# Kernel tuning notes

Measured on AMD Instinct MI355X. Metric: run time of the kernel, lower is better.

The kernel has to match this reference:

```python
import jax, jax.numpy as jnp
import numpy as np

NB_STEPS = 50  # quadrature steps (51 Clenshaw-Curtis nodes)
IN_D = 8
HIDDEN = [256, 256, 256]
B = 8192


def _cc_quadrature(nb_steps):
    # Clenshaw-Curtis weights/nodes, exactly as in UMNN's ParallelNeuralIntegral
    lam = np.arange(nb_steps + 1).reshape(-1, 1)
    lam = np.cos((lam @ lam.T) * np.pi / nb_steps)
    lam[:, 0] = 0.5
    lam[:, -1] = 0.5 * lam[:, -1]
    lam = lam * 2.0 / nb_steps
    W = np.arange(nb_steps + 1).reshape(-1, 1)
    W[np.arange(1, nb_steps + 1, 2)] = 0
    W = 2.0 / (1 - W.astype(np.float64) ** 2)
    W[0] = 1.0
    W[np.arange(1, nb_steps + 1, 2)] = 0.0
    cc_weights = (lam.T @ W).astype(np.float32)  # [S+1, 1]
    steps = np.cos(np.arange(nb_steps + 1).reshape(-1, 1) * np.pi / nb_steps).astype(np.float32)  # [S+1,1]
    return jnp.asarray(cc_weights), jnp.asarray(steps)


def setup_inputs() -> dict:
    key = jax.random.key(0)
    ks = jax.random.split(key, 20)
    inp = {
        "x": jax.random.normal(ks[0], (B, 1), dtype=jnp.float32),
        "h": jax.random.normal(ks[1], (B, IN_D - 1), dtype=jnp.float32),
    }
    # integrand net: in_d -> 256 -> 256 -> 256 -> 1
    i_dims = [IN_D] + HIDDEN + [1]
    for li, (d0, d1) in enumerate(zip(i_dims, i_dims[1:])):
        scale = 1.0 / np.sqrt(d0)
        inp[f"iW{li}"] = jax.random.uniform(ks[2 + li], (d0, d1), jnp.float32, -scale, scale)
        inp[f"ib{li}"] = jax.random.uniform(ks[6 + li], (d1,), jnp.float32, -scale, scale)
    # h net: (in_d-1) -> 256 -> 256 -> 256 -> 2
    h_dims = [IN_D - 1] + HIDDEN + [2]
    for li, (d0, d1) in enumerate(zip(h_dims, h_dims[1:])):
        scale = 1.0 / np.sqrt(d0)
        inp[f"hW{li}"] = jax.random.uniform(ks[10 + li], (d0, d1), jnp.float32, -scale, scale)
        inp[f"hb{li}"] = jax.random.uniform(ks[14 + li], (d1,), jnp.float32, -scale, scale)
    return inp


def _integrand(z, Ws, bs):
    # IntegrandNN: Linear+ReLU chain, final Linear+ELU, then +1
    for W, b in zip(Ws[:-1], bs[:-1]):
        z = jax.nn.relu(z @ W + b)
    return jax.nn.elu(z @ Ws[-1] + bs[-1]) + 1.0


def _hnet(z, Ws, bs):
    # Linear+ReLU chain, final Linear (ReLU popped)
    for W, b in zip(Ws[:-1], bs[:-1]):
        z = jax.nn.relu(z @ W + b)
    return z @ Ws[-1] + bs[-1]


def _forward(x, h, iWs, ibs, hWs, hbs):
    cc_w, steps = _cc_quadrature(NB_STEPS)  # [S,1], [S,1]
    S = NB_STEPS + 1
    b = x.shape[0]
    # quadrature nodes mapped from [-1,1] to [0, x] (x0 = 0)
    X = x[:, None, :] * (steps[None, :, :] + 1.0) * 0.5          # [B,S,1]
    Hs = jnp.broadcast_to(h[:, None, :], (b, S, h.shape[1]))     # [B,S,in_d-1]
    z = jnp.concatenate([X, Hs], axis=-1)                        # [B,S,in_d]
    dz = _integrand(z, iWs, ibs)                                 # [B,S,1]
    integral = jnp.sum(dz * cc_w[None, :, :], axis=1) * x * 0.5  # [B,1]
    out = _hnet(h, hWs, hbs)                                     # [B,2]
    offset = out[:, :1]
    scaling = jnp.exp(out[:, 1:2])
    return scaling * integral + offset


def reference(x, h, iW0, ib0, iW1, ib1, iW2, ib2, iW3, ib3,
              hW0, hb0, hW1, hb1, hW2, hb2, hW3, hb3):
    iWs = [iW0, iW1, iW2, iW3]
    ibs = [ib0, ib1, ib2, ib3]
    hWs = [hW0, hW1, hW2, hW3]
    hbs = [hb0, hb1, hb2, hb3]
    return _forward(x, h, iWs, ibs, hWs, hbs)
```

## Files before the change

### kernel.cpp

```cpp
#include <hip/hip_runtime.h>
#include <hip/hip_bf16.h>
#include <math.h>

using bf16x8 = __attribute__((ext_vector_type(8))) __bf16;
using f32x16 = __attribute__((ext_vector_type(16))) float;

#define B_SZ    8192
#define S_STEPS 51
#define M_ROWS  (B_SZ * S_STEPS)
#define TROWS   64

__device__ __forceinline__ f32x16 mfma32(bf16x8 a, bf16x8 b, f32x16 c) {
    return __builtin_amdgcn_mfma_f32_32x32x16_bf16(a, b, c, 0, 0, 0);
}

__global__ void ccq_kernel(float* __restrict__ ccw, float* __restrict__ stp) {
    int s = threadIdx.x;
    if (s >= S_STEPS) return;
    double pi50 = M_PI / 50.0;
    double acc = 0.0;
    for (int j = 0; j <= 50; j += 2) {
        double wq = (j == 0) ? 1.0 : 2.0 / (1.0 - (double)(j * j));
        double m;
        if (s == 0) m = 0.5;
        else if (s == 50) m = 0.5;
        else m = cos((double)(j * s) * pi50);
        acc += m * wq;
    }
    ccw[s] = (float)(acc * (2.0 / 50.0));
    stp[s] = (float)cos((double)s * pi50);
}

struct PackArgs {
    const float* src[8];
    __hip_bfloat16* dst[8];
    int Ks[8], Ns[8], KST[8], perm[8];
    int prefix[9];
};

__global__ void pack_all(PackArgs pa) {
    int idx = blockIdx.x * 256 + threadIdx.x;
    if (idx >= pa.prefix[8]) return;
    int m = 0;
    while (idx >= pa.prefix[m + 1]) ++m;
    int e = idx - pa.prefix[m];
    int KST = pa.KST[m];
    int j    = e & 7;
    int lane = (e >> 3) & 63;
    int ks   = (e >> 9) % KST;
    int cg   = (e >> 9) / KST;
    int col = cg * 32 + (lane & 31);
    int k   = ks * 16 + (lane >> 5) * 8 + j;
    int kk  = pa.perm[m] ? ((k & ~63) | (((k & 63) >> 1) + 32 * (k & 1))) : k;
    float v = (kk < pa.Ks[m] && col < pa.Ns[m]) ? pa.src[m][kk * pa.Ns[m] + col] : 0.0f;
    ((__bf16*)pa.dst[m])[e] = (__bf16)v;
}


template<int KST, int CHUNKS, int MASK>
__device__ __forceinline__ void gemm_compute(const __bf16* __restrict__ actIn,
                                             const __bf16* __restrict__ wpack,
                                             f32x16 (&acc)[2][2],
                                             int wc, int lane) {
    const bf16x8* wp = (const bf16x8*)wpack;
    const int la = lane & 31, hi = lane >> 5;
#pragma unroll 4
    for (int ks = 0; ks < KST; ++ks) {
        bf16x8 b0 = wp[((wc * 2 + 0) * KST + ks) * 64 + lane];
        bf16x8 b1 = wp[((wc * 2 + 1) * KST + ks) * 64 + lane];
        int chunk = ks * 2 + hi;
#pragma unroll
        for (int m = 0; m < 2; ++m) {
            int row = m * 32 + la;
            bf16x8 af = *(const bf16x8*)(actIn + (row * CHUNKS + (chunk ^ (row & MASK))) * 8);
            acc[m][0] = mfma32(af, b0, acc[m][0]);
            acc[m][1] = mfma32(af, b1, acc[m][1]);
        }
    }
}

__device__ __forceinline__ void epilogue_store(f32x16 (&acc)[2][2],
                                               const float* __restrict__ bias,
                                               __bf16* __restrict__ actOut,
                                               int wc, int lane) {
    const int la = lane & 31, hi = lane >> 5;
    unsigned* dst = (unsigned*)actOut;
    int F = wc * 64 + la;
    float b0 = bias[F], b1 = bias[F + 32];
    int d = wc * 32 + la;
    int c = d >> 2, w = d & 3;
#pragma unroll
    for (int m = 0; m < 2; ++m) {
#pragma unroll
        for (int r = 0; r < 16; ++r) {
            int row = m * 32 + (r & 3) + 8 * (r >> 2) + 4 * hi;
            float v0 = fmaxf(acc[m][0][r] + b0, 0.0f);
            float v1 = fmaxf(acc[m][1][r] + b1, 0.0f);
            union { __bf16 h2[2]; unsigned u; } cv;
            cv.h2[0] = (__bf16)v0; cv.h2[1] = (__bf16)v1;
            dst[(row * 32 + (c ^ (row & 31))) * 4 + w] = cv.u;
        }
    }
}

template<int MODE>
__device__ __forceinline__ void final_layer(const __bf16* __restrict__ actIn,
                                            const __bf16* __restrict__ wpack,
                                            const float* __restrict__ bias,
                                            float* __restrict__ out0,
                                            float* __restrict__ out1,
                                            int rb, int wid, int lane) {
    const bf16x8* wp = (const bf16x8*)wpack;
    const int la = lane & 31, hi = lane >> 5;
    f32x16 acc = (f32x16)0.0f;
    int row = wid * 32 + la;
#pragma unroll 4
    for (int ks = 0; ks < 16; ++ks) {
        int chunk = ks * 2 + hi;
        bf16x8 af = *(const bf16x8*)(actIn + (row * 32 + (chunk ^ (row & 31))) * 8);
        acc = mfma32(af, wp[ks * 64 + lane], acc);
    }
    if (MODE == 0) {
        if (la == 0) {
            float b = bias[0];
#pragma unroll
            for (int r = 0; r < 16; ++r) {
                int rr = wid * 32 + (r & 3) + 8 * (r >> 2) + 4 * hi;
                float v = acc[r] + b;
                out0[rb + rr] = (v > 0.0f) ? (v + 1.0f) : expf(v);
            }
        }
    } else {
        if (la < 2) {
            float b = bias[la];
            float* dst = (la == 0) ? out0 : out1;
#pragma unroll
            for (int r = 0; r < 16; ++r) {
                int rr = wid * 32 + (r & 3) + 8 * (r >> 2) + 4 * hi;
                dst[rb + rr] = acc[r] + b;
            }
        }
    }
}

template<int MODE>
__global__ __launch_bounds__(256, 4) void mlp_kernel(
    const float* __restrict__ x, const float* __restrict__ h,
    const float* __restrict__ steps,
    const __bf16* __restrict__ w0p, const __bf16* __restrict__ w1p,
    const __bf16* __restrict__ w2p, const __bf16* __restrict__ w3p,
    const float* __restrict__ b0, const float* __restrict__ b1,
    const float* __restrict__ b2, const float* __restrict__ b3,
    float* __restrict__ out0, float* __restrict__ out1) {
    __shared__ __bf16 act[TROWS * 256];
    __shared__ __bf16 zin[TROWS * 32];

    int tid  = threadIdx.x;
    int lane = tid & 63;
    int wid  = tid >> 6;
    int wc   = wid;
    int rb   = blockIdx.x * TROWS;

    {
        int row   = tid >> 2;
        int cpart = tid & 3;
        float vals[8];
        if (MODE == 0) {
            int s  = rb >> 13;
            int i  = (rb & (B_SZ - 1)) + row;
            float sc = (steps[s] + 1.0f) * 0.5f;
#pragma unroll
            for (int j = 0; j < 8; ++j) {
                int c = cpart * 8 + j;
                float v = 0.0f;
                if (c == 0) v = x[i] * sc;
                else if (c < 8) v = h[i * 7 + c - 1];
                vals[j] = v;
            }
        } else {
            int i = rb + row;
#pragma unroll
            for (int j = 0; j < 8; ++j) {
                int c = cpart * 8 + j;
                vals[j] = (c < 7) ? h[i * 7 + c] : 0.0f;
            }
        }
        bf16x8 zv;
#pragma unroll
        for (int j = 0; j < 8; ++j) zv[j] = (__bf16)vals[j];
        int zidx = (row * 4 + (cpart ^ (row & 3))) * 8;
        *(bf16x8*)(zin + zidx) = zv;
    }
    __syncthreads();

    f32x16 acc[2][2];

#pragma unroll
    for (int m = 0; m < 2; ++m)
#pragma unroll
        for (int n = 0; n < 2; ++n) acc[m][n] = (f32x16)0.0f;
    gemm_compute<2, 4, 3>(zin, w0p, acc, wc, lane);
    epilogue_store(acc, b0, act, wc, lane);
    __syncthreads();

#pragma unroll
    for (int m = 0; m < 2; ++m)
#pragma unroll
        for (int n = 0; n < 2; ++n) acc[m][n] = (f32x16)0.0f;
    gemm_compute<16, 32, 31>(act, w1p, acc, wc, lane);
    __syncthreads();
    epilogue_store(acc, b1, act, wc, lane);
    __syncthreads();

#pragma unroll
    for (int m = 0; m < 2; ++m)
#pragma unroll
        for (int n = 0; n < 2; ++n) acc[m][n] = (f32x16)0.0f;
    gemm_compute<16, 32, 31>(act, w2p, acc, wc, lane);
    __syncthreads();
    epilogue_store(acc, b2, act, wc, lane);
    __syncthreads();

    if (wid < 2)
        final_layer<MODE>(act, w3p, b3, out0, out1, rb, wid, lane);
}

__global__ void reduce_kernel(const float* __restrict__ dz, const float* __restrict__ x,
                              const float* __restrict__ ho, const float* __restrict__ hs,
                              const float* __restrict__ ccw, float* __restrict__ out) {
    __shared__ float w[S_STEPS];
    int t = threadIdx.x;
    if (t < S_STEPS) w[t] = ccw[t];
    __syncthreads();
    int i = blockIdx.x * blockDim.x + t;
    float acc = 0.0f;
    for (int s = 0; s < S_STEPS; ++s) acc += dz[s * B_SZ + i] * w[s];
    float integral = acc * x[i] * 0.5f;
    out[i] = expf(hs[i]) * integral + ho[i];
}

extern "C" void kernel_launch(void* const* d_in, const int* in_sizes, int n_in,
                              void* d_out, int out_size, void* d_ws, size_t ws_size,
                              hipStream_t stream) {
    (void)in_sizes; (void)n_in; (void)out_size; (void)ws_size;
    const float* x = (const float*)d_in[0];
    const float* h = (const float*)d_in[1];
    const float* iW[4] = {(const float*)d_in[2], (const float*)d_in[4],
                          (const float*)d_in[6], (const float*)d_in[8]};
    const float* ib[4] = {(const float*)d_in[3], (const float*)d_in[5],
                          (const float*)d_in[7], (const float*)d_in[9]};
    const float* hW[4] = {(const float*)d_in[10], (const float*)d_in[12],
                          (const float*)d_in[14], (const float*)d_in[16]};
    const float* hb[4] = {(const float*)d_in[11], (const float*)d_in[13],
                          (const float*)d_in[15], (const float*)d_in[17]};

    size_t off = 0;
    auto alloc = [&](size_t bytes) -> void* {
        void* p = (char*)d_ws + off;
        off += (bytes + 255) & ~(size_t)255;
        return p;
    };
    float*  dz   = (float*)alloc((size_t)M_ROWS * 4);
    float*  ho   = (float*)alloc(B_SZ * 4);
    float*  hs   = (float*)alloc(B_SZ * 4);
    float*  ccw  = (float*)alloc(64 * 4);
    float*  stp  = (float*)alloc(64 * 4);
    __bf16* iW0p = (__bf16*)alloc(8 * 2 * 512 * 2);
    __bf16* iW1p = (__bf16*)alloc(8 * 16 * 512 * 2);
    __bf16* iW2p = (__bf16*)alloc(8 * 16 * 512 * 2);
    __bf16* iW3p = (__bf16*)alloc(1 * 16 * 512 * 2);
    __bf16* hW0p = (__bf16*)alloc(8 * 2 * 512 * 2);
    __bf16* hW1p = (__bf16*)alloc(8 * 16 * 512 * 2);
    __bf16* hW2p = (__bf16*)alloc(8 * 16 * 512 * 2);
    __bf16* hW3p = (__bf16*)alloc(1 * 16 * 512 * 2);

    ccq_kernel<<<1, 64, 0, stream>>>(ccw, stp);

    PackArgs pa;
    const float* srcs[8] = {iW[0], iW[1], iW[2], iW[3], hW[0], hW[1], hW[2], hW[3]};
    __bf16*      dsts[8] = {iW0p, iW1p, iW2p, iW3p, hW0p, hW1p, hW2p, hW3p};
    int Ks[8]  = {8, 256, 256, 256, 7, 256, 256, 256};
    int Ns[8]  = {256, 256, 256, 1, 256, 256, 256, 2};
    int KST[8] = {2, 16, 16, 16, 2, 16, 16, 16};
    int CG[8]  = {8, 8, 8, 1, 8, 8, 8, 1};
    int PM[8]  = {0, 1, 1, 1, 0, 1, 1, 1};
    int pfx = 0;
    for (int m = 0; m < 8; ++m) {
        pa.src[m] = srcs[m];
        pa.dst[m] = (__hip_bfloat16*)dsts[m];
        pa.Ks[m] = Ks[m]; pa.Ns[m] = Ns[m]; pa.KST[m] = KST[m]; pa.perm[m] = PM[m];
        pa.prefix[m] = pfx;
        pfx += CG[m] * KST[m] * 512;
    }
    pa.prefix[8] = pfx;
    pack_all<<<(pfx + 255) / 256, 256, 0, stream>>>(pa);

    mlp_kernel<0><<<M_ROWS / TROWS, 256, 0, stream>>>(
        x, h, stp, iW0p, iW1p, iW2p, iW3p, ib[0], ib[1], ib[2], ib[3], dz, dz);
    mlp_kernel<1><<<B_SZ / TROWS, 256, 0, stream>>>(
        x, h, stp, hW0p, hW1p, hW2p, hW3p, hb[0], hb[1], hb[2], hb[3], ho, hs);

    reduce_kernel<<<B_SZ / 256, 256, 0, stream>>>(dz, x, ho, hs, ccw, (float*)d_out);
}
```

Measured before the change: 163.3 us.

## Load first-layer inputs directly into MFMA registers and precompute LDS swizzle offsets

The first layer no longer stages its inputs through a shared-memory tile. Each lane now loads x and h straight from global memory into bf16 MFMA fragments, and the layer uses a single K-step, which removes one barrier and the zin buffer. The hidden-layer GEMM and epilogue address shared memory through precomputed byte offsets with an XOR swizzle, the k-loop is fully unrolled, and wave priority is raised around the MFMA loop. The aim is less address arithmetic, fewer LDS round trips and better MFMA issue, at the cost of more registers and half the lanes sitting idle during the layer-0 load.

```diff
diff --git a/kernel.cpp b/kernel.cpp
--- a/kernel.cpp
+++ b/kernel.cpp
@@ -57,26 +57,66 @@
 }
 
 
-template<int KST, int CHUNKS, int MASK>
+template<int KST>
 __device__ __forceinline__ void gemm_compute(const __bf16* __restrict__ actIn,
                                              const __bf16* __restrict__ wpack,
                                              f32x16 (&acc)[2][2],
                                              int wc, int lane) {
     const bf16x8* wp = (const bf16x8*)wpack;
     const int la = lane & 31, hi = lane >> 5;
-#pragma unroll 4
+    const char* base = (const char*)actIn;
+    const int C0 = la * 512 + ((hi ^ (la & 1)) << 4);
+    const int D  = (la & 30) << 4;
+    __builtin_amdgcn_s_setprio(1);
+#pragma unroll
     for (int ks = 0; ks < KST; ++ks) {
         bf16x8 b0 = wp[((wc * 2 + 0) * KST + ks) * 64 + lane];
         bf16x8 b1 = wp[((wc * 2 + 1) * KST + ks) * 64 + lane];
-        int chunk = ks * 2 + hi;
-#pragma unroll
-        for (int m = 0; m < 2; ++m) {
+        const int kv = ks << 5;
+        bf16x8 a0 = *(const bf16x8*)(base + C0 + (kv ^ D));
+        bf16x8 a1 = *(const bf16x8*)(base + C0 + 16384 + (kv ^ D));
+        acc[0][0] = mfma32(a0, b0, acc[0][0]);
+        acc[0][1] = mfma32(a0, b1, acc[0][1]);
+        acc[1][0] = mfma32(a1, b0, acc[1][0]);
+        acc[1][1] = mfma32(a1, b1, acc[1][1]);
+    }
+    __builtin_amdgcn_s_setprio(0);
+}
+
+template<int MODE>
+__device__ __forceinline__ void l0_compute(const float* __restrict__ x,
+                                           const float* __restrict__ h,
+                                           float sc,
+                                           const __bf16* __restrict__ w0p,
+                                           f32x16 (&acc)[2][2],
+                                           int rb, int wc, int lane) {
+    const bf16x8* wp = (const bf16x8*)w0p;
+    const int la = lane & 31, hi = lane >> 5;
+    bf16x8 a[2];
+#pragma unroll
+    for (int m = 0; m < 2; ++m) {
+        bf16x8 v = (bf16x8)(__bf16)0.0f;
+        if (hi == 0) {
             int row = m * 32 + la;
-            bf16x8 af = *(const bf16x8*)(actIn + (row * CHUNKS + (chunk ^ (row & MASK))) * 8);
-            acc[m][0] = mfma32(af, b0, acc[m][0]);
-            acc[m][1] = mfma32(af, b1, acc[m][1]);
+            int i = (MODE == 0) ? ((rb & (B_SZ - 1)) + row) : (rb + row);
+            const float* hp = h + i * 7;
+            if (MODE == 0) {
+                v[0] = (__bf16)(x[i] * sc);
+#pragma unroll
+                for (int j = 0; j < 7; ++j) v[j + 1] = (__bf16)hp[j];
+            } else {
+#pragma unroll
+                for (int j = 0; j < 7; ++j) v[j] = (__bf16)hp[j];
+            }
         }
-    }
+        a[m] = v;
+    }
+    bf16x8 b0 = wp[(wc * 2 + 0) * 64 + lane];
+    bf16x8 b1 = wp[(wc * 2 + 1) * 64 + lane];
+    acc[0][0] = mfma32(a[0], b0, acc[0][0]);
+    acc[0][1] = mfma32(a[0], b1, acc[0][1]);
+    acc[1][0] = mfma32(a[1], b0, acc[1][0]);
+    acc[1][1] = mfma32(a[1], b1, acc[1][1]);
 }
 
 __device__ __forceinline__ void epilogue_store(f32x16 (&acc)[2][2],
@@ -84,21 +124,22 @@
                                                __bf16* __restrict__ actOut,
                                                int wc, int lane) {
     const int la = lane & 31, hi = lane >> 5;
-    unsigned* dst = (unsigned*)actOut;
+    char* dst = (char*)actOut;
     int F = wc * 64 + la;
-    float b0 = bias[F], b1 = bias[F + 32];
+    float b0v = bias[F], b1v = bias[F + 32];
     int d = wc * 32 + la;
-    int c = d >> 2, w = d & 3;
+    const int cH4 = ((d >> 2) ^ (hi << 2)) << 4;
+    const int P   = hi * 2048 + ((d & 3) << 2);
 #pragma unroll
     for (int m = 0; m < 2; ++m) {
 #pragma unroll
         for (int r = 0; r < 16; ++r) {
-            int row = m * 32 + (r & 3) + 8 * (r >> 2) + 4 * hi;
-            float v0 = fmaxf(acc[m][0][r] + b0, 0.0f);
-            float v1 = fmaxf(acc[m][1][r] + b1, 0.0f);
+            const int K_r = (r & 3) + 8 * (r >> 2);
+            float v0 = fmaxf(acc[m][0][r] + b0v, 0.0f);
+            float v1 = fmaxf(acc[m][1][r] + b1v, 0.0f);
             union { __bf16 h2[2]; unsigned u; } cv;
             cv.h2[0] = (__bf16)v0; cv.h2[1] = (__bf16)v1;
-            dst[(row * 32 + (c ^ (row & 31))) * 4 + w] = cv.u;
+            *(unsigned*)(dst + P + m * 16384 + K_r * 512 + (cH4 ^ (K_r << 4))) = cv.u;
         }
     }
 }
@@ -112,12 +153,13 @@
                                             int rb, int wid, int lane) {
     const bf16x8* wp = (const bf16x8*)wpack;
     const int la = lane & 31, hi = lane >> 5;
+    const char* base = (const char*)actIn;
+    const int C = (wid * 32 + la) * 512 + ((hi ^ (la & 1)) << 4);
+    const int D = (la & 30) << 4;
     f32x16 acc = (f32x16)0.0f;
-    int row = wid * 32 + la;
-#pragma unroll 4
+#pragma unroll
     for (int ks = 0; ks < 16; ++ks) {
-        int chunk = ks * 2 + hi;
-        bf16x8 af = *(const bf16x8*)(actIn + (row * 32 + (chunk ^ (row & 31))) * 8);
+        bf16x8 af = *(const bf16x8*)(base + C + ((ks << 5) ^ D));
         acc = mfma32(af, wp[ks * 64 + lane], acc);
     }
     if (MODE == 0) {
@@ -153,7 +195,6 @@
     const float* __restrict__ b2, const float* __restrict__ b3,
     float* __restrict__ out0, float* __restrict__ out1) {
     __shared__ __bf16 act[TROWS * 256];
-    __shared__ __bf16 zin[TROWS * 32];
 
     int tid  = threadIdx.x;
     int lane = tid & 63;
@@ -161,37 +202,8 @@
     int wc   = wid;
     int rb   = blockIdx.x * TROWS;
 
-    {
-        int row   = tid >> 2;
-        int cpart = tid & 3;
-        float vals[8];
-        if (MODE == 0) {
-            int s  = rb >> 13;
-            int i  = (rb & (B_SZ - 1)) + row;
-            float sc = (steps[s] + 1.0f) * 0.5f;
-#pragma unroll
-            for (int j = 0; j < 8; ++j) {
-                int c = cpart * 8 + j;
-                float v = 0.0f;
-                if (c == 0) v = x[i] * sc;
-                else if (c < 8) v = h[i * 7 + c - 1];
-                vals[j] = v;
-            }
-        } else {
-            int i = rb + row;
-#pragma unroll
-            for (int j = 0; j < 8; ++j) {
-                int c = cpart * 8 + j;
-                vals[j] = (c < 7) ? h[i * 7 + c] : 0.0f;
-            }
-        }
-        bf16x8 zv;
-#pragma unroll
-        for (int j = 0; j < 8; ++j) zv[j] = (__bf16)vals[j];
-        int zidx = (row * 4 + (cpart ^ (row & 3))) * 8;
-        *(bf16x8*)(zin + zidx) = zv;
-    }
-    __syncthreads();
+    float sc = 0.0f;
+    if (MODE == 0) sc = (steps[rb >> 13] + 1.0f) * 0.5f;
 
     f32x16 acc[2][2];
 
@@ -199,7 +211,7 @@
     for (int m = 0; m < 2; ++m)
 #pragma unroll
         for (int n = 0; n < 2; ++n) acc[m][n] = (f32x16)0.0f;
-    gemm_compute<2, 4, 3>(zin, w0p, acc, wc, lane);
+    l0_compute<MODE>(x, h, sc, w0p, acc, rb, wc, lane);
     epilogue_store(acc, b0, act, wc, lane);
     __syncthreads();
 
@@ -207,7 +219,7 @@
     for (int m = 0; m < 2; ++m)
 #pragma unroll
         for (int n = 0; n < 2; ++n) acc[m][n] = (f32x16)0.0f;
-    gemm_compute<16, 32, 31>(act, w1p, acc, wc, lane);
+    gemm_compute<16>(act, w1p, acc, wc, lane);
     __syncthreads();
     epilogue_store(acc, b1, act, wc, lane);
     __syncthreads();
@@ -216,7 +228,7 @@
     for (int m = 0; m < 2; ++m)
 #pragma unroll
         for (int n = 0; n < 2; ++n) acc[m][n] = (f32x16)0.0f;
-    gemm_compute<16, 32, 31>(act, w2p, acc, wc, lane);
+    gemm_compute<16>(act, w2p, acc, wc, lane);
     __syncthreads();
     epilogue_store(acc, b2, act, wc, lane);
     __syncthreads();
@@ -265,11 +277,11 @@
     float*  hs   = (float*)alloc(B_SZ * 4);
     float*  ccw  = (float*)alloc(64 * 4);
     float*  stp  = (float*)alloc(64 * 4);
-    __bf16* iW0p = (__bf16*)alloc(8 * 2 * 512 * 2);
+    __bf16* iW0p = (__bf16*)alloc(8 * 1 * 512 * 2);
     __bf16* iW1p = (__bf16*)alloc(8 * 16 * 512 * 2);
     __bf16* iW2p = (__bf16*)alloc(8 * 16 * 512 * 2);
     __bf16* iW3p = (__bf16*)alloc(1 * 16 * 512 * 2);
-    __bf16* hW0p = (__bf16*)alloc(8 * 2 * 512 * 2);
+    __bf16* hW0p = (__bf16*)alloc(8 * 1 * 512 * 2);
     __bf16* hW1p = (__bf16*)alloc(8 * 16 * 512 * 2);
     __bf16* hW2p = (__bf16*)alloc(8 * 16 * 512 * 2);
     __bf16* hW3p = (__bf16*)alloc(1 * 16 * 512 * 2);
@@ -281,7 +293,7 @@
     __bf16*      dsts[8] = {iW0p, iW1p, iW2p, iW3p, hW0p, hW1p, hW2p, hW3p};
     int Ks[8]  = {8, 256, 256, 256, 7, 256, 256, 256};
     int Ns[8]  = {256, 256, 256, 1, 256, 256, 256, 2};
-    int KST[8] = {2, 16, 16, 16, 2, 16, 16, 16};
+    int KST[8] = {1, 16, 16, 16, 1, 16, 16, 16};
     int CG[8]  = {8, 8, 8, 1, 8, 8, 8, 1};
     int PM[8]  = {0, 1, 1, 1, 0, 1, 1, 1};
     int pfx = 0;
```

Measured after the change: 157.6 us. 1.04x faster.
